# Kernel tuning notes

Measured on AMD Instinct MI355X. Metric: run time of the kernel, lower is better.

## Reference

```python
import jax, jax.numpy as jnp
import numpy as np

B, S, E, H = 2, 2048, 1024, 16
DK = E // H


def setup_inputs() -> dict:
    key = jax.random.key(0)
    ks = jax.random.split(key, 8)
    scale = 1.0 / np.sqrt(E)
    inp = {
        "query": jax.random.normal(ks[0], (B, S, E), jnp.float32),
        "key": jax.random.normal(ks[1], (B, S, E), jnp.float32),
        "value": jax.random.normal(ks[2], (B, S, E), jnp.float32),
        # causal mask: True = masked out (upper triangle)
        "attn_mask": jnp.triu(jnp.ones((S, S), jnp.bool_), k=1),
        "Wq": jax.random.normal(ks[3], (E, E), jnp.float32) * scale,
        "bq": jnp.zeros((E,), jnp.float32),
        "Wk": jax.random.normal(ks[4], (E, E), jnp.float32) * scale,
        "bk": jnp.zeros((E,), jnp.float32),
        "Wv": jax.random.normal(ks[5], (E, E), jnp.float32) * scale,
        "bv": jnp.zeros((E,), jnp.float32),
        "Wo": jax.random.normal(ks[6], (E, E), jnp.float32) * scale,
        "bo": jnp.zeros((E,), jnp.float32),
    }
    return inp


def reference(query, key, value, attn_mask, Wq, bq, Wk, bk, Wv, bv, Wo, bo):
    bs = query.shape[0]
    # QKV projections, split heads: [B,S,E] -> [B,H,S,DK]
    def proj(x, W, b):
        y = jnp.einsum('bse,ef->bsf', x, W) + b
        return y.reshape(bs, -1, H, DK).transpose(0, 2, 1, 3)

    q = proj(query, Wq, bq)
    k = proj(key, Wk, bk)
    v = proj(value, Wv, bv)

    # scaled dot-product attention with additive -1e9 mask fill
    scores = jnp.einsum('bhqd,bhkd->bhqk', q, k) / np.sqrt(DK).astype(jnp.float32)
    scores = jnp.where(attn_mask[None, None, :, :], jnp.float32(-1e9), scores)
    attn = jax.nn.softmax(scores, axis=-1)
    ctx = jnp.einsum('bhqk,bhkd->bhqd', attn, v)  # [B,H,S,DK]

    concat = ctx.transpose(0, 2, 1, 3).reshape(bs, -1, E)  # [B,S,E]
    return jnp.einsum('bse,ef->bsf', concat, Wo) + bo
```

## Files before the change

kernel.cpp:

```cpp
#include <hip/hip_runtime.h>
#include <hip/hip_bf16.h>

typedef __attribute__((ext_vector_type(8))) short bf16x8;
typedef __attribute__((ext_vector_type(4))) float f32x4;

constexpr int Bc = 2, Sc = 2048, Ec = 1024, Hc = 16, DKc = 64;

__device__ __forceinline__ unsigned short f2b(float f) {
    union { float f; unsigned u; } v; v.f = f;
    unsigned u = v.u;
    return (unsigned short)((u + 0x7FFFu + ((u >> 16) & 1u)) >> 16);
}
__device__ __forceinline__ float b2f(unsigned short h) {
    union { unsigned u; float f; } v; v.u = ((unsigned)h) << 16;
    return v.f;
}

#define GLOAD16(ldsp, gp)                                                                  \
    __builtin_amdgcn_global_load_lds((const __attribute__((address_space(1))) void*)(gp),  \
                                     (__attribute__((address_space(3))) void*)(ldsp),      \
                                     16, 0, 0)

#define ASM_VM4 asm volatile("s_waitcnt vmcnt(4)" ::: "memory")
#define ASM_VM0 asm volatile("s_waitcnt vmcnt(0)" ::: "memory")
#define ASM_LG0 asm volatile("s_waitcnt lgkmcnt(0)" ::: "memory")
#define ASM_BAR asm volatile("s_barrier" ::: "memory")

__global__ __launch_bounds__(256) void conv_x(
    const float* __restrict__ Xq, const float* __restrict__ Xk, const float* __restrict__ Xv,
    unsigned short* __restrict__ Xb)
{
    const int z = blockIdx.y;
    const float* X = (z == 0) ? Xq : (z == 1) ? Xk : Xv;
    unsigned short* O = Xb + (size_t)z * 4194304;
    const int n4 = 4194304 / 4;
    for (int i = blockIdx.x * 256 + threadIdx.x; i < n4; i += gridDim.x * 256) {
        float4 v = ((const float4*)X)[i];
        ushort4 h; h.x = f2b(v.x); h.y = f2b(v.y); h.z = f2b(v.z); h.w = f2b(v.w);
        ((ushort4*)O)[i] = h;
    }
}

__global__ __launch_bounds__(256) void conv_w(
    const float* __restrict__ Wq, const float* __restrict__ Wk,
    const float* __restrict__ Wv, const float* __restrict__ Wo,
    unsigned short* __restrict__ Wt)
{
    const int z = blockIdx.z;
    const float* W = (z == 0) ? Wq : (z == 1) ? Wk : (z == 2) ? Wv : Wo;
    unsigned short* O = Wt + (size_t)z * 1048576;
    __shared__ unsigned short T[64][65];
    const int k0 = blockIdx.y * 64, n0 = blockIdx.x * 64;
    const int tx = threadIdx.x & 15, ty = threadIdx.x >> 4;
    #pragma unroll
    for (int p = 0; p < 4; p++) {
        float4 v = *(const float4*)&W[(size_t)(k0 + ty + 16 * p) * 1024 + n0 + 4 * tx];
        T[ty + 16 * p][4 * tx + 0] = f2b(v.x);
        T[ty + 16 * p][4 * tx + 1] = f2b(v.y);
        T[ty + 16 * p][4 * tx + 2] = f2b(v.z);
        T[ty + 16 * p][4 * tx + 3] = f2b(v.w);
    }
    __syncthreads();
    #pragma unroll
    for (int p = 0; p < 4; p++) {
        ushort4 o;
        o.x = T[4 * tx + 0][ty + 16 * p];
        o.y = T[4 * tx + 1][ty + 16 * p];
        o.z = T[4 * tx + 2][ty + 16 * p];
        o.w = T[4 * tx + 3][ty + 16 * p];
        *(ushort4*)&O[(size_t)(n0 + ty + 16 * p) * 1024 + k0 + 4 * tx] = o;
    }
}

#define GEMM_STAGE(buf, kk)                                                                \
    _Pragma("unroll")                                                                      \
    for (int i = 0; i < 2; i++) {                                                          \
        const int rb = 32 * w + 16 * i;                                                    \
        GLOAD16(SMEM[buf] + rb * 32, Ag + (size_t)(m0 + rb + lr) * 1024 + (kk) + lcs);     \
        GLOAD16(SMEM[2 + (buf)] + rb * 32, Bg + (size_t)(n0 + rb + lr) * 1024 + (kk) + lcs); \
    }

#define GEMM_CORE_CV                                                                       \
    GEMM_STAGE(0, 0)                                                                       \
    GEMM_STAGE(1, 32)                                                                      \
    for (int t = 0; t < 32; t++) {                                                         \
        const int cur = t & 1;                                                             \
        if (t < 31) { ASM_VM4; } else { ASM_VM0; }                                         \
        ASM_BAR;                                                                           \
        bf16x8 a[4], b[4];                                                                 \
        _Pragma("unroll")                                                                  \
        for (int m = 0; m < 4; m++)                                                        \
            a[m] = *(const bf16x8*)((const char*)SMEM[cur] +                               \
                   (wr + 16 * m + c) * 64 + ((g ^ ((c >> 1) & 3)) << 4));                  \
        _Pragma("unroll")                                                                  \
        for (int n = 0; n < 4; n++)                                                        \
            b[n] = *(const bf16x8*)((const char*)SMEM[2 + cur] +                           \
                   (wc + 16 * n + c) * 64 + ((g ^ ((c >> 1) & 3)) << 4));                  \
        ASM_LG0;                                                                           \
        ASM_BAR;                                                                           \
        if (t + 2 < 32) { GEMM_STAGE(cur, (t + 2) * 32) }                                  \
        __builtin_amdgcn_s_setprio(1);                                                     \
        _Pragma("unroll")                                                                  \
        for (int m = 0; m < 4; m++)                                                        \
            _Pragma("unroll")                                                              \
            for (int n = 0; n < 4; n++)                                                    \
                acc[m][n] = __builtin_amdgcn_mfma_f32_16x16x32_bf16(a[m], b[n], acc[m][n], 0, 0, 0); \
        __builtin_amdgcn_s_setprio(0);                                                     \
    }

__global__ __launch_bounds__(256) void gemm_qkv(
    const unsigned short* __restrict__ Xb, const unsigned short* __restrict__ Wt,
    const float* __restrict__ bq, const float* __restrict__ bk, const float* __restrict__ bv,
    unsigned short* __restrict__ Qw, unsigned short* __restrict__ Kw,
    unsigned short* __restrict__ Vt)
{
    const int wgid = blockIdx.x;
    const int xcd = wgid & 7, slot = wgid >> 3;
    const int y = xcd + 8 * (slot & 3);
    const int xz = slot >> 2;
    const int x = xz & 7, z = xz >> 3;

    const unsigned short* Ag = Xb + (size_t)z * 4194304;
    const unsigned short* Bg = Wt + (size_t)z * 1048576;
    const float* bias = (z == 0) ? bq : (z == 1) ? bk : bv;

    __shared__ __align__(16) unsigned short SMEM[4][4096];

    const int tid = threadIdx.x;
    const int m0 = y * 128, n0 = x * 128;
    const int lane = tid & 63, c = lane & 15, g = lane >> 4;
    const int w = tid >> 6;
    const int wr = (w >> 1) * 64, wc = (w & 1) * 64;
    const int lr = lane >> 2;
    const int lcs = ((lane & 3) ^ ((lane >> 3) & 3)) * 8;

    f32x4 acc[4][4] = {};
    GEMM_CORE_CV

    if (z == 2) {
        unsigned short* Tr = &SMEM[0][0];
        #pragma unroll
        for (int n = 0; n < 4; n++) {
            const int dl = wc + n * 16 + c;
            const float bv_ = bias[n0 + dl];
            #pragma unroll
            for (int m = 0; m < 4; m++) {
                const int sl = wr + m * 16 + 4 * g;
                ushort4 pw;
                pw.x = f2b(acc[m][n][0] + bv_);
                pw.y = f2b(acc[m][n][1] + bv_);
                pw.z = f2b(acc[m][n][2] + bv_);
                pw.w = f2b(acc[m][n][3] + bv_);
                const int sc = (sl >> 2) ^ (dl & 7);
                *(ushort4*)&Tr[dl * 128 + sc * 4] = pw;
            }
        }
        ASM_BAR;
        #pragma unroll
        for (int it = 0; it < 16; it++) {
            const int idx = it * 256 + tid;
            const int dl = idx >> 5;
            const int sc0 = idx & 31;
            const int sc = sc0 ^ (dl & 7);
            const ushort4 pw = *(const ushort4*)&Tr[dl * 128 + sc * 4];
            const int gn = n0 + dl;
            const int h = gn >> 6, d = gn & 63;
            const int gm = m0 + sc0 * 4;
            const int bb = gm >> 11, s = gm & 2047;
            *(ushort4*)&Vt[((size_t)(bb * Hc + h) * DKc + d) * Sc + s] = pw;
        }
    } else {
        #pragma unroll
        for (int n = 0; n < 4; n++) {
            const int gn = n0 + wc + n * 16 + c;
            const float bv_ = bias[gn];
            const int h = gn >> 6, d = gn & 63;
            #pragma unroll
            for (int m = 0; m < 4; m++) {
                #pragma unroll
                for (int r = 0; r < 4; r++) {
                    const int gm = m0 + wr + m * 16 + 4 * g + r;
                    const int bb = gm >> 11, s = gm & 2047;
                    const float val = acc[m][n][r] + bv_;
                    if (z == 0)
                        Qw[((size_t)(bb * Hc + h) * Sc + s) * DKc + d] = f2b(val * 0.125f);
                    else
                        Kw[((size_t)(bb * Hc + h) * Sc + s) * DKc + d] = f2b(val);
                }
            }
        }
    }
}

__global__ __launch_bounds__(256) void gemm_out(
    const unsigned short* __restrict__ Ctx, const unsigned short* __restrict__ Wt,
    const float* __restrict__ bo, float* __restrict__ Out)
{
    const int wgid = blockIdx.x;
    const int xcd = wgid & 7, slot = wgid >> 3;
    const int y = xcd + 8 * (slot & 3);
    const int x = slot >> 2;

    const unsigned short* Ag = Ctx;
    const unsigned short* Bg = Wt + (size_t)3 * 1048576;

    __shared__ __align__(16) unsigned short SMEM[4][4096];

    const int tid = threadIdx.x;
    const int m0 = y * 128, n0 = x * 128;
    const int lane = tid & 63, c = lane & 15, g = lane >> 4;
    const int w = tid >> 6;
    const int wr = (w >> 1) * 64, wc = (w & 1) * 64;
    const int lr = lane >> 2;
    const int lcs = ((lane & 3) ^ ((lane >> 3) & 3)) * 8;

    f32x4 acc[4][4] = {};
    GEMM_CORE_CV

    #pragma unroll
    for (int n = 0; n < 4; n++) {
        const int gn = n0 + wc + n * 16 + c;
        const float bv_ = bo[gn];
        #pragma unroll
        for (int m = 0; m < 4; m++) {
            #pragma unroll
            for (int r = 0; r < 4; r++) {
                const int gm = m0 + wr + m * 16 + 4 * g + r;
                Out[(size_t)gm * Ec + gn] = acc[m][n][r] + bv_;
            }
        }
    }
}

__global__ __launch_bounds__(256) void attn(
    const unsigned short* __restrict__ Qw, const unsigned short* __restrict__ Kw,
    const unsigned short* __restrict__ Vt,
    unsigned short* __restrict__ Opart, float* __restrict__ Lpart)
{
    const int bid = blockIdx.x;
    const int bh = bid & 31;
    const int ps = bid >> 5;
    const int pair = ps >> 1, sp = ps & 1;
    const int tid = threadIdx.x, w = tid >> 6, lane = tid & 63;
    const int c = lane & 15, g = lane >> 4;

    const unsigned short* Qh = Qw + (size_t)bh * Sc * DKc;
    const unsigned short* Kh = Kw + (size_t)bh * Sc * DKc;
    const unsigned short* Vh = Vt + (size_t)bh * DKc * Sc;

    __shared__ __align__(16) unsigned short Kl[2][4096];
    __shared__ __align__(16) unsigned short Vl[2][4096];
    __shared__ __align__(16) unsigned short Pl[4][16][72];

    const int lrow8 = lane >> 3;
    const int cbp = ((lane & 7) ^ lrow8) << 4;
    const int swz = (c & 7) << 4;

#define STAGE_KV(BUF, KV0)                                                                  \
    _Pragma("unroll")                                                                       \
    for (int s2 = 0; s2 < 2; s2++) {                                                        \
        const int row_ = s2 * 32 + w * 8 + lrow8;                                           \
        GLOAD16((char*)Kl[BUF] + s2 * 4096 + w * 1024,                                      \
                (const char*)Kh + (size_t)((KV0) + row_) * 128 + cbp);                      \
        GLOAD16((char*)Vl[BUF] + s2 * 4096 + w * 1024,                                      \
                (const char*)Vh + (size_t)row_ * 4096 + (size_t)(KV0) * 2 + cbp);           \
    }

    for (int half = 0; half < 2; half++) {
        const int qt = half ? (31 - pair) : pair;
        const int qbase = qt * 64;
        const int qrow = qbase + w * 16 + c;
        const int qtg = bh * 32 + qt;

        const bf16x8 q0 = *(const bf16x8*)&Qh[(size_t)qrow * DKc + 8 * g];
        const bf16x8 q1 = *(const bf16x8*)&Qh[(size_t)qrow * DKc + 32 + 8 * g];

        float lsum = 0.f;
        f32x4 o[4] = {};

        int buf = 0;
        STAGE_KV(0, sp * 64)
        __syncthreads();

        for (int j = sp; j <= qt; j += 2) {
            const int kv0 = j * 64;
            const bool maskt = (j == qt);

            if (j + 2 <= qt) { STAGE_KV(buf ^ 1, (j + 2) * 64) }

            f32x4 d[4] = {};
            __builtin_amdgcn_s_setprio(1);
            #pragma unroll
            for (int t = 0; t < 4; t++) {
                const char* kb = (const char*)Kl[buf] + (16 * t + c) * 128;
                const bf16x8 k0 = *(const bf16x8*)(kb + ((16 * g) ^ swz));
                const bf16x8 k1 = *(const bf16x8*)(kb + ((64 + 16 * g) ^ swz));
                d[t] = __builtin_amdgcn_mfma_f32_16x16x32_bf16(k0, q0, d[t], 0, 0, 0);
                d[t] = __builtin_amdgcn_mfma_f32_16x16x32_bf16(k1, q1, d[t], 0, 0, 0);
            }
            __builtin_amdgcn_s_setprio(0);

            float s[16];
            if (maskt) {
                #pragma unroll
                for (int t = 0; t < 4; t++)
                    #pragma unroll
                    for (int r = 0; r < 4; r++) {
                        const int kv = kv0 + 16 * t + 4 * g + r;
                        s[4 * t + r] = __expf((kv <= qrow) ? d[t][r] : -1e30f);
                    }
            } else {
                #pragma unroll
                for (int t = 0; t < 4; t++)
                    #pragma unroll
                    for (int r = 0; r < 4; r++)
                        s[4 * t + r] = __expf(d[t][r]);
            }
            #pragma unroll
            for (int i = 0; i < 16; i++) lsum += s[i];

            #pragma unroll
            for (int t = 0; t < 4; t++) {
                ushort4 pw;
                pw.x = f2b(s[4 * t + 0]); pw.y = f2b(s[4 * t + 1]);
                pw.z = f2b(s[4 * t + 2]); pw.w = f2b(s[4 * t + 3]);
                *(ushort4*)&Pl[w][c][16 * t + 4 * g] = pw;
            }
            const bf16x8 pA0 = *(const bf16x8*)&Pl[w][c][8 * g];
            const bf16x8 pA1 = *(const bf16x8*)&Pl[w][c][32 + 8 * g];

            __builtin_amdgcn_s_setprio(1);
            #pragma unroll
            for (int ch = 0; ch < 4; ch++) {
                const char* vb = (const char*)Vl[buf] + (16 * ch + c) * 128;
                const bf16x8 v0 = *(const bf16x8*)(vb + ((16 * g) ^ swz));
                const bf16x8 v1 = *(const bf16x8*)(vb + ((64 + 16 * g) ^ swz));
                f32x4 t = o[ch];
                t = __builtin_amdgcn_mfma_f32_16x16x32_bf16(pA0, v0, t, 0, 0, 0);
                o[ch] = __builtin_amdgcn_mfma_f32_16x16x32_bf16(pA1, v1, t, 0, 0, 0);
            }
            __builtin_amdgcn_s_setprio(0);
            __syncthreads();
            buf ^= 1;
        }

        lsum += __shfl_xor(lsum, 16);
        lsum += __shfl_xor(lsum, 32);
        if (g == 0)
            Lpart[((size_t)sp * 1024 + qtg) * 64 + w * 16 + c] = lsum;

        #pragma unroll
        for (int ch = 0; ch < 4; ch++) {
            #pragma unroll
            for (int r = 0; r < 4; r++) {
                const int lrow = w * 16 + 4 * g + r;
                Opart[(((size_t)sp * 1024 + qtg) * 64 + lrow) * 64 + ch * 16 + c] =
                    f2b(o[ch][r]);
            }
        }
    }
#undef STAGE_KV
}

__global__ __launch_bounds__(256) void attn_combine(
    const unsigned short* __restrict__ Opart, const float* __restrict__ Lpart,
    unsigned short* __restrict__ Ctx)
{
    const int qtg = blockIdx.x;
    const int bh = qtg >> 5, qt = qtg & 31;
    const int bb = bh >> 4, hh = bh & 15;
    #pragma unroll
    for (int it = 0; it < 2; it++) {
        const int chunk = threadIdx.x + it * 256;
        const int row = chunk >> 3, c8 = (chunk & 7) * 8;
        const size_t o0 = ((size_t)qtg * 64 + row) * 64 + c8;
        const size_t o1 = ((size_t)(1024 + qtg) * 64 + row) * 64 + c8;
        const bf16x8 a = *(const bf16x8*)&Opart[o0];
        const bf16x8 b = *(const bf16x8*)&Opart[o1];
        const float linv = 1.f / (Lpart[(size_t)qtg * 64 + row] +
                                  Lpart[(size_t)(1024 + qtg) * 64 + row]);
        ushort4 lo, hi;
        lo.x = f2b((b2f((unsigned short)a[0]) + b2f((unsigned short)b[0])) * linv);
        lo.y = f2b((b2f((unsigned short)a[1]) + b2f((unsigned short)b[1])) * linv);
        lo.z = f2b((b2f((unsigned short)a[2]) + b2f((unsigned short)b[2])) * linv);
        lo.w = f2b((b2f((unsigned short)a[3]) + b2f((unsigned short)b[3])) * linv);
        hi.x = f2b((b2f((unsigned short)a[4]) + b2f((unsigned short)b[4])) * linv);
        hi.y = f2b((b2f((unsigned short)a[5]) + b2f((unsigned short)b[5])) * linv);
        hi.z = f2b((b2f((unsigned short)a[6]) + b2f((unsigned short)b[6])) * linv);
        hi.w = f2b((b2f((unsigned short)a[7]) + b2f((unsigned short)b[7])) * linv);
        const int qg = qt * 64 + row;
        unsigned short* dst = &Ctx[((size_t)(bb * Sc + qg)) * Ec + hh * 64 + c8];
        *(ushort4*)dst = lo;
        *(ushort4*)(dst + 4) = hi;
    }
}

extern "C" void kernel_launch(void* const* d_in, const int* in_sizes, int n_in,
                              void* d_out, int out_size, void* d_ws, size_t ws_size,
                              hipStream_t stream) {
    const float* query = (const float*)d_in[0];
    const float* key   = (const float*)d_in[1];
    const float* value = (const float*)d_in[2];
    const float* Wq = (const float*)d_in[4];
    const float* bq = (const float*)d_in[5];
    const float* Wk = (const float*)d_in[6];
    const float* bk = (const float*)d_in[7];
    const float* Wv = (const float*)d_in[8];
    const float* bv = (const float*)d_in[9];
    const float* Wo = (const float*)d_in[10];
    const float* bo = (const float*)d_in[11];

    const size_t n_elem = (size_t)Bc * Hc * Sc * DKc;
    unsigned short* Qw = (unsigned short*)d_ws;
    unsigned short* Kw = Qw + n_elem;
    unsigned short* Vt = Kw + n_elem;
    unsigned short* Cx = Vt + n_elem;
    unsigned short* Xb = Cx + n_elem;
    unsigned short* Wt = Xb + 3 * n_elem;

    unsigned short* Opart = Xb;
    float* Lpart = (float*)(Xb + (size_t)2 * 1024 * 64 * 64);

    conv_x<<<dim3(512, 3), 256, 0, stream>>>(query, key, value, Xb);
    conv_w<<<dim3(16, 16, 4), 256, 0, stream>>>(Wq, Wk, Wv, Wo, Wt);
    gemm_qkv<<<dim3(768), 256, 0, stream>>>(Xb, Wt, bq, bk, bv, Qw, Kw, Vt);
    attn<<<dim3(1024), 256, 0, stream>>>(Qw, Kw, Vt, Opart, Lpart);
    attn_combine<<<dim3(1024), 256, 0, stream>>>(Opart, Lpart, Cx);
    gemm_out<<<dim3(256), 256, 0, stream>>>(Cx, Wt, bo, (float*)d_out);
}
```

Baseline: 116.5 us.

## Triple-buffer GEMM loads, single-buffer attention KV, use intrinsic bf16 conversion

```diff
diff --git a/kernel.cpp b/kernel.cpp
--- a/kernel.cpp
+++ b/kernel.cpp
@@ -11,6 +11,9 @@
     unsigned u = v.u;
     return (unsigned short)((u + 0x7FFFu + ((u >> 16) & 1u)) >> 16);
 }
+__device__ __forceinline__ unsigned short f2bn(float f) {
+    return __bfloat16_as_ushort(__float2bfloat16(f));
+}
 __device__ __forceinline__ float b2f(unsigned short h) {
     union { unsigned u; float f; } v; v.u = ((unsigned)h) << 16;
     return v.f;
@@ -21,6 +24,7 @@
                                      (__attribute__((address_space(3))) void*)(ldsp),      \
                                      16, 0, 0)
 
+#define ASM_VM8 asm volatile("s_waitcnt vmcnt(8)" ::: "memory")
 #define ASM_VM4 asm volatile("s_waitcnt vmcnt(4)" ::: "memory")
 #define ASM_VM0 asm volatile("s_waitcnt vmcnt(0)" ::: "memory")
 #define ASM_LG0 asm volatile("s_waitcnt lgkmcnt(0)" ::: "memory")
@@ -77,15 +81,16 @@
     for (int i = 0; i < 2; i++) {                                                          \
         const int rb = 32 * w + 16 * i;                                                    \
         GLOAD16(SMEM[buf] + rb * 32, Ag + (size_t)(m0 + rb + lr) * 1024 + (kk) + lcs);     \
-        GLOAD16(SMEM[2 + (buf)] + rb * 32, Bg + (size_t)(n0 + rb + lr) * 1024 + (kk) + lcs); \
+        GLOAD16(SMEM[3 + (buf)] + rb * 32, Bg + (size_t)(n0 + rb + lr) * 1024 + (kk) + lcs); \
     }
 
 #define GEMM_CORE_CV                                                                       \
     GEMM_STAGE(0, 0)                                                                       \
     GEMM_STAGE(1, 32)                                                                      \
+    GEMM_STAGE(2, 64)                                                                      \
     for (int t = 0; t < 32; t++) {                                                         \
-        const int cur = t & 1;                                                             \
-        if (t < 31) { ASM_VM4; } else { ASM_VM0; }                                         \
+        const int cur = t % 3;                                                             \
+        if (t < 30) { ASM_VM8; } else if (t == 30) { ASM_VM4; } else { ASM_VM0; }          \
         ASM_BAR;                                                                           \
         bf16x8 a[4], b[4];                                                                 \
         _Pragma("unroll")                                                                  \
@@ -94,11 +99,11 @@
                    (wr + 16 * m + c) * 64 + ((g ^ ((c >> 1) & 3)) << 4));                  \
         _Pragma("unroll")                                                                  \
         for (int n = 0; n < 4; n++)                                                        \
-            b[n] = *(const bf16x8*)((const char*)SMEM[2 + cur] +                           \
+            b[n] = *(const bf16x8*)((const char*)SMEM[3 + cur] +                           \
                    (wc + 16 * n + c) * 64 + ((g ^ ((c >> 1) & 3)) << 4));                  \
         ASM_LG0;                                                                           \
         ASM_BAR;                                                                           \
-        if (t + 2 < 32) { GEMM_STAGE(cur, (t + 2) * 32) }                                  \
+        if (t + 3 < 32) { GEMM_STAGE(cur, (t + 3) * 32) }                                  \
         __builtin_amdgcn_s_setprio(1);                                                     \
         _Pragma("unroll")                                                                  \
         for (int m = 0; m < 4; m++)                                                        \
@@ -124,7 +129,7 @@
     const unsigned short* Bg = Wt + (size_t)z * 1048576;
     const float* bias = (z == 0) ? bq : (z == 1) ? bk : bv;
 
-    __shared__ __align__(16) unsigned short SMEM[4][4096];
+    __shared__ __align__(16) unsigned short SMEM[6][4096];
 
     const int tid = threadIdx.x;
     const int m0 = y * 128, n0 = x * 128;
@@ -139,6 +144,7 @@
 
     if (z == 2) {
         unsigned short* Tr = &SMEM[0][0];
+        ASM_BAR;
         #pragma unroll
         for (int n = 0; n < 4; n++) {
             const int dl = wc + n * 16 + c;
@@ -204,7 +210,7 @@
     const unsigned short* Ag = Ctx;
     const unsigned short* Bg = Wt + (size_t)3 * 1048576;
 
-    __shared__ __align__(16) unsigned short SMEM[4][4096];
+    __shared__ __align__(16) unsigned short SMEM[6][4096];
 
     const int tid = threadIdx.x;
     const int m0 = y * 128, n0 = x * 128;
@@ -248,21 +254,21 @@
     const unsigned short* Kh = Kw + (size_t)bh * Sc * DKc;
     const unsigned short* Vh = Vt + (size_t)bh * DKc * Sc;
 
-    __shared__ __align__(16) unsigned short Kl[2][4096];
-    __shared__ __align__(16) unsigned short Vl[2][4096];
+    __shared__ __align__(16) unsigned short Kl[4096];
+    __shared__ __align__(16) unsigned short Vl[4096];
     __shared__ __align__(16) unsigned short Pl[4][16][72];
 
     const int lrow8 = lane >> 3;
     const int cbp = ((lane & 7) ^ lrow8) << 4;
     const int swz = (c & 7) << 4;
 
-#define STAGE_KV(BUF, KV0)                                                                  \
+#define STAGE_KV(KV0)                                                                       \
     _Pragma("unroll")                                                                       \
     for (int s2 = 0; s2 < 2; s2++) {                                                        \
         const int row_ = s2 * 32 + w * 8 + lrow8;                                           \
-        GLOAD16((char*)Kl[BUF] + s2 * 4096 + w * 1024,                                      \
+        GLOAD16((char*)Kl + s2 * 4096 + w * 1024,                                           \
                 (const char*)Kh + (size_t)((KV0) + row_) * 128 + cbp);                      \
-        GLOAD16((char*)Vl[BUF] + s2 * 4096 + w * 1024,                                      \
+        GLOAD16((char*)Vl + s2 * 4096 + w * 1024,                                           \
                 (const char*)Vh + (size_t)row_ * 4096 + (size_t)(KV0) * 2 + cbp);           \
     }
 
@@ -278,21 +284,18 @@
         float lsum = 0.f;
         f32x4 o[4] = {};
 
-        int buf = 0;
-        STAGE_KV(0, sp * 64)
-        __syncthreads();
-
         for (int j = sp; j <= qt; j += 2) {
             const int kv0 = j * 64;
             const bool maskt = (j == qt);
 
-            if (j + 2 <= qt) { STAGE_KV(buf ^ 1, (j + 2) * 64) }
+            STAGE_KV(kv0)
+            __syncthreads();
 
             f32x4 d[4] = {};
             __builtin_amdgcn_s_setprio(1);
             #pragma unroll
             for (int t = 0; t < 4; t++) {
-                const char* kb = (const char*)Kl[buf] + (16 * t + c) * 128;
+                const char* kb = (const char*)Kl + (16 * t + c) * 128;
                 const bf16x8 k0 = *(const bf16x8*)(kb + ((16 * g) ^ swz));
                 const bf16x8 k1 = *(const bf16x8*)(kb + ((64 + 16 * g) ^ swz));
                 d[t] = __builtin_amdgcn_mfma_f32_16x16x32_bf16(k0, q0, d[t], 0, 0, 0);
@@ -322,8 +325,8 @@
             #pragma unroll
             for (int t = 0; t < 4; t++) {
                 ushort4 pw;
-                pw.x = f2b(s[4 * t + 0]); pw.y = f2b(s[4 * t + 1]);
-                pw.z = f2b(s[4 * t + 2]); pw.w = f2b(s[4 * t + 3]);
+                pw.x = f2bn(s[4 * t + 0]); pw.y = f2bn(s[4 * t + 1]);
+                pw.z = f2bn(s[4 * t + 2]); pw.w = f2bn(s[4 * t + 3]);
                 *(ushort4*)&Pl[w][c][16 * t + 4 * g] = pw;
             }
             const bf16x8 pA0 = *(const bf16x8*)&Pl[w][c][8 * g];
@@ -332,7 +335,7 @@
             __builtin_amdgcn_s_setprio(1);
             #pragma unroll
             for (int ch = 0; ch < 4; ch++) {
-                const char* vb = (const char*)Vl[buf] + (16 * ch + c) * 128;
+                const char* vb = (const char*)Vl + (16 * ch + c) * 128;
                 const bf16x8 v0 = *(const bf16x8*)(vb + ((16 * g) ^ swz));
                 const bf16x8 v1 = *(const bf16x8*)(vb + ((64 + 16 * g) ^ swz));
                 f32x4 t = o[ch];
@@ -341,7 +344,6 @@
             }
             __builtin_amdgcn_s_setprio(0);
             __syncthreads();
-            buf ^= 1;
         }
 
         lsum += __shfl_xor(lsum, 16);
@@ -355,7 +357,7 @@
             for (int r = 0; r < 4; r++) {
                 const int lrow = w * 16 + 4 * g + r;
                 Opart[(((size_t)sp * 1024 + qtg) * 64 + lrow) * 64 + ch * 16 + c] =
-                    f2b(o[ch][r]);
+                    f2bn(o[ch][r]);
             }
         }
     }
@@ -380,14 +382,14 @@
         const float linv = 1.f / (Lpart[(size_t)qtg * 64 + row] +
                                   Lpart[(size_t)(1024 + qtg) * 64 + row]);
         ushort4 lo, hi;
-        lo.x = f2b((b2f((unsigned short)a[0]) + b2f((unsigned short)b[0])) * linv);
-        lo.y = f2b((b2f((unsigned short)a[1]) + b2f((unsigned short)b[1])) * linv);
-        lo.z = f2b((b2f((unsigned short)a[2]) + b2f((unsigned short)b[2])) * linv);
-        lo.w = f2b((b2f((unsigned short)a[3]) + b2f((unsigned short)b[3])) * linv);
-        hi.x = f2b((b2f((unsigned short)a[4]) + b2f((unsigned short)b[4])) * linv);
-        hi.y = f2b((b2f((unsigned short)a[5]) + b2f((unsigned short)b[5])) * linv);
-        hi.z = f2b((b2f((unsigned short)a[6]) + b2f((unsigned short)b[6])) * linv);
-        hi.w = f2b((b2f((unsigned short)a[7]) + b2f((unsigned short)b[7])) * linv);
+        lo.x = f2bn((b2f((unsigned short)a[0]) + b2f((unsigned short)b[0])) * linv);
+        lo.y = f2bn((b2f((unsigned short)a[1]) + b2f((unsigned short)b[1])) * linv);
+        lo.z = f2bn((b2f((unsigned short)a[2]) + b2f((unsigned short)b[2])) * linv);
+        lo.w = f2bn((b2f((unsigned short)a[3]) + b2f((unsigned short)b[3])) * linv);
+        hi.x = f2bn((b2f((unsigned short)a[4]) + b2f((unsigned short)b[4])) * linv);
+        hi.y = f2bn((b2f((unsigned short)a[5]) + b2f((unsigned short)b[5])) * linv);
+        hi.z = f2bn((b2f((unsigned short)a[6]) + b2f((unsigned short)b[6])) * linv);
+        hi.w = f2bn((b2f((unsigned short)a[7]) + b2f((unsigned short)b[7])) * linv);
         const int qg = qt * 64 + row;
         unsigned short* dst = &Ctx[((size_t)(bb * Sc + qg)) * Ec + hh * 64 + c8];
         *(ushort4*)dst = lo;
```

Result: faster. 109.8 us (-5.7%).
